# Kernel optimization log

Measured on AMD Instinct MI355X. Metric: run time of the kernel, lower is better.

The kernel has to match this reference:

```python
import jax, jax.numpy as jnp
import numpy as np

B, M, D, H = 2, 2048, 1024, 16
DH = D // H            # 64 head dim
R_ATTN = 512           # rank of q/k/v SVD factors
FFN_D = 2048           # GEGLU inner dim; Wi out = 2*FFN_D
R_FFN = 1024           # rank of FFN SVD factors
ROPE_BASE = 10000.0
LN_EPS = 1e-5


def _layernorm(x, g, b):
    mu = jnp.mean(x, axis=-1, keepdims=True)
    var = jnp.mean(jnp.square(x - mu), axis=-1, keepdims=True)
    return (x - mu) * jax.lax.rsqrt(var + LN_EPS) * g + b


def _rotate_half(x):
    x1, x2 = jnp.split(x, 2, axis=-1)
    return jnp.concatenate((-x2, x1), axis=-1)


def _rope_cos_sin(m, dh, dtype):
    inv_freq = 1.0 / (ROPE_BASE ** (jnp.arange(0, dh, 2, dtype=jnp.float32) / dh))
    freqs = jnp.arange(m, dtype=jnp.float32)[:, None] * inv_freq[None, :]  # [M, dh/2]
    emb = jnp.concatenate((freqs, freqs), axis=-1)  # [M, dh]
    return jnp.cos(emb).astype(dtype), jnp.sin(emb).astype(dtype)


def setup_inputs() -> dict:
    key = jax.random.key(0)
    ks = iter(jax.random.split(key, 32))
    rn = lambda shape, s: jax.random.normal(next(ks), shape, jnp.float32) * s
    w = 0.02
    return {
        'hidden_states': rn((B, M, D), 1.0),
        'ln1_g': jnp.ones((D,), jnp.float32), 'ln1_b': jnp.zeros((D,), jnp.float32),
        'Uq': rn((D, R_ATTN), w), 'Vq': rn((R_ATTN, D), w), 'bq': rn((D,), w),
        'Uk': rn((D, R_ATTN), w), 'Vk': rn((R_ATTN, D), w), 'bk': rn((D,), w),
        'Uv': rn((D, R_ATTN), w), 'Vv': rn((R_ATTN, D), w), 'bv': rn((D,), w),
        'Wo': rn((D, D), w), 'bo': rn((D,), w),  # dense attn out proj, torch [out,in]
        'ln2_g': jnp.ones((D,), jnp.float32), 'ln2_b': jnp.zeros((D,), jnp.float32),
        'U1': rn((D, R_FFN), w), 'V1': rn((R_FFN, 2 * FFN_D), w), 'b1': rn((2 * FFN_D,), w),
        'U2': rn((FFN_D, R_FFN), w), 'V2': rn((R_FFN, D), w), 'b2': rn((D,), w),
    }


def reference(hidden_states, ln1_g, ln1_b, Uq, Vq, bq, Uk, Vk, bk, Uv, Vv, bv,
              Wo, bo, ln2_g, ln2_b, U1, V1, b1, U2, V2, b2):
    x = hidden_states
    xn = _layernorm(x, ln1_g, ln1_b)
    # low-rank QKV: y = (x @ U) @ V + b
    q = (xn @ Uq) @ Vq + bq
    k = (xn @ Uk) @ Vk + bk
    v = (xn @ Uv) @ Vv + bv
    to_bhmd = lambda t: t.reshape(B, M, H, DH).transpose(0, 2, 1, 3)
    q, k, v = to_bhmd(q), to_bhmd(k), to_bhmd(v)
    cos, sin = _rope_cos_sin(M, DH, q.dtype)  # [M, DH]
    q = q * cos + _rotate_half(q) * sin
    k = k * cos + _rotate_half(k) * sin
    scale = 1.0 / np.sqrt(DH)
    scores = jnp.einsum('bhmd,bhnd->bhmn', q, k) * scale  # [B,H,M,M]
    attn = jax.nn.softmax(scores, axis=-1)
    out = jnp.einsum('bhmn,bhnd->bhmd', attn, v)
    out = out.transpose(0, 2, 1, 3).reshape(B, M, D)
    x = x + out @ Wo.T + bo
    # low-rank GEGLU FFN
    xn2 = _layernorm(x, ln2_g, ln2_b)
    z = (xn2 @ U1) @ V1 + b1  # [B,M,2*FFN_D]
    z1, z2 = jnp.split(z, 2, axis=-1)
    h = jax.nn.gelu(z1, approximate=True) * z2  # GEGLU, tanh approx
    y = (h @ U2) @ V2 + b2
    return x + y
```

## Files before the change

kernel.cpp:

```cpp
#include <hip/hip_runtime.h>


typedef unsigned short u16;
typedef unsigned int u32;
typedef u16 u16x8 __attribute__((ext_vector_type(8)));
typedef __bf16 bf16x8 __attribute__((ext_vector_type(8)));
typedef float f32x4 __attribute__((ext_vector_type(4)));

__device__ __forceinline__ u16 f2bf(float f) {
    u32 u = __builtin_bit_cast(u32, f);
    u += 0x7fff + ((u >> 16) & 1);
    return (u16)(u >> 16);
}
__device__ __forceinline__ float bf2f(u16 h) {
    u32 u = ((u32)h) << 16;
    return __builtin_bit_cast(float, u);
}
__device__ __forceinline__ u32 packbf(float a, float b) {
    return __builtin_amdgcn_perm(__builtin_bit_cast(u32, b),
                                 __builtin_bit_cast(u32, a), 0x07060302u);
}

__device__ __forceinline__ void gload16(const void* g, void* l) {
    __builtin_amdgcn_global_load_lds(
        (const __attribute__((address_space(1))) void*)g,
        (__attribute__((address_space(3))) void*)l, 16, 0, 0);
}

#define MB 1048576u
#define OFF_UQKVT (0*MB)
#define OFF_VQKVT (3*MB)
#define OFF_WOB   (6*MB)
#define OFF_U1T   (8*MB)
#define OFF_V1TP  (10*MB)
#define OFF_U2T   (18*MB)
#define OFF_V2T   (22*MB)
#define OFF_BQKV  (24*MB)
#define OFF_B1P   (24*MB + 16384u)
#define OFF_XN    (25*MB)
#define OFF_TBUF  (33*MB)
#define OFF_QB    (45*MB)
#define OFF_KB    (53*MB)
#define OFF_HB    (45*MB)
#define OFF_VTB   (61*MB)
#define OFF_OB    (69*MB)
#define OFF_X2    (93*MB)

__global__ __launch_bounds__(256) void prep_kernel(
    const float* __restrict__ Uq, const float* __restrict__ Uk,
    const float* __restrict__ Uv, const float* __restrict__ Vq,
    const float* __restrict__ Vk, const float* __restrict__ Vv,
    const float* __restrict__ Wo, const float* __restrict__ U1,
    const float* __restrict__ V1, const float* __restrict__ U2,
    const float* __restrict__ V2,
    const float* __restrict__ bq, const float* __restrict__ bk,
    const float* __restrict__ bv, const float* __restrict__ b1,
    u16* __restrict__ UQKVT, u16* __restrict__ VQKVT, u16* __restrict__ WOB,
    u16* __restrict__ U1T, u16* __restrict__ V1TP, u16* __restrict__ U2T,
    u16* __restrict__ V2T, float* __restrict__ BQKV, float* __restrict__ B1P)
{
    __shared__ float tile[32][33];
    int bid = blockIdx.x;

    if (bid >= 12288) {
        int id = (bid - 12288) * 256 + threadIdx.x;
        if (id < 3072) {
            float v = (id < 1024) ? bq[id] : (id < 2048 ? bk[id - 1024] : bv[id - 2048]);
            BQKV[id] = v;
        }
        int g = id >> 5, s = id & 31;
        B1P[id] = b1[(s < 16) ? (g*16 + s) : (2048 + g*16 + (s - 16))];
        return;
    }
    if (bid >= 11264) {
        int i4 = ((bid - 11264) * 256 + threadIdx.x) * 4;
        float4 v = *(const float4*)(Wo + i4);
        u16 tmp[4] = {f2bf(v.x), f2bf(v.y), f2bf(v.z), f2bf(v.w)};
        *(uint2*)(WOB + i4) = *(const uint2*)tmp;
        return;
    }

    const float* src; u16* dst; int K, N, src_ld, nx; bool gg = false;
    if (bid < 3072) {
        int t = bid / 512; bid -= t * 512;
        if (t < 3) { src = t==0 ? Uq : (t==1 ? Uk : Uv);
                     dst = UQKVT + t * 512*1024; K = 1024; N = 512; src_ld = 512; nx = 16; }
        else { int z = t - 3; src = z==0 ? Vq : (z==1 ? Vk : Vv);
               dst = VQKVT + z * 524288; K = 512; N = 1024; src_ld = 1024; nx = 32; }
    } else if (bid < 4096)  { src = U1; dst = U1T;  K = 1024; N = 1024; src_ld = 1024; nx = 32;  bid -= 3072; }
    else if (bid < 8192)    { src = V1; dst = V1TP; K = 1024; N = 4096; src_ld = 4096; nx = 128; bid -= 4096; gg = true; }
    else if (bid < 10240)   { src = U2; dst = U2T;  K = 2048; N = 1024; src_ld = 1024; nx = 32;  bid -= 8192; }
    else                    { src = V2; dst = V2T;  K = 1024; N = 1024; src_ld = 1024; nx = 32;  bid -= 10240; }

    int tx = threadIdx.x & 31, ty = threadIdx.x >> 5;
    int n0 = (bid % nx) * 32, k0 = (bid / nx) * 32;
    int srccol;
    if (gg) { int g = n0 >> 5; srccol = (tx < 16) ? (g*16 + tx) : (2048 + g*16 + (tx - 16)); }
    else srccol = n0 + tx;
    for (int i = 0; i < 4; i++)
        tile[ty + i*8][tx] = src[(size_t)(k0 + ty + i*8) * src_ld + srccol];
    __syncthreads();
    for (int i = 0; i < 4; i++)
        dst[(size_t)(n0 + ty + i*8) * K + k0 + tx] = f2bf(tile[tx][ty + i*8]);
}

__global__ __launch_bounds__(256) void ln_kernel(
    const float* __restrict__ x, const float* __restrict__ g,
    const float* __restrict__ bta, u16* __restrict__ out)
{
    int w = threadIdx.x >> 6, lane = threadIdx.x & 63;
    int row = blockIdx.x * 4 + w;
    const float* xr = x + (size_t)row * 1024;
    float vals[16];
    float s = 0.f, s2 = 0.f;
    #pragma unroll
    for (int ii = 0; ii < 16; ii++) {
        float v = xr[lane + ii*64];
        vals[ii] = v; s += v; s2 += v * v;
    }
    #pragma unroll
    for (int off = 1; off < 64; off <<= 1) {
        s  += __shfl_xor(s, off);
        s2 += __shfl_xor(s2, off);
    }
    float mu = s * (1.f/1024.f);
    float var = s2 * (1.f/1024.f) - mu * mu;
    float rs = rsqrtf(var + 1e-5f);
    #pragma unroll
    for (int ii = 0; ii < 16; ii++) {
        int col = lane + ii*64;
        out[(size_t)row * 1024 + col] = f2bf((vals[ii] - mu) * rs * g[col] + bta[col]);
    }
}

__global__ __launch_bounds__(256) void gemm_bt_kernel(
    const u16* __restrict__ A, int lda, const u16* __restrict__ Bt,
    void* __restrict__ Cout, int ldc, const float* __restrict__ bias,
    const float* __restrict__ resid, int Kdim, int mode)
{
    __shared__ u16 As[2][4096];
    __shared__ u16 Bs[2][4096];
    int tid = threadIdx.x;
    int m0 = blockIdx.y * 128, n0 = blockIdx.x * 128;
    int w = tid >> 6, lane = tid & 63, quad = lane >> 4, l15 = lane & 15;
    int wm = (w >> 1) * 64, wn = (w & 1) * 64;
    int sr = tid >> 2, sc8 = (tid & 3) * 8;

    f32x4 acc[4][4] = {};

    const u16* Ap = A  + (size_t)(m0 + sr) * lda  + sc8;
    const u16* Bp = Bt + (size_t)(n0 + sr) * Kdim + sc8;

    #define GSTAGE(buf, koff) do {                                        \
        gload16(Ap + (koff),                     &As[buf][tid * 8]);      \
        gload16(Ap + (koff) + (size_t)64 * lda,  &As[buf][2048 + tid*8]); \
        gload16(Bp + (koff),                     &Bs[buf][tid * 8]);      \
        gload16(Bp + (koff) + (size_t)64 * Kdim, &Bs[buf][2048 + tid*8]); \
    } while (0)

    GSTAGE(0, 0);
    __syncthreads();

    for (int k0 = 0; k0 < Kdim; k0 += 32) {
        int cur = (k0 >> 5) & 1;
        if (k0 + 32 < Kdim) GSTAGE(cur ^ 1, k0 + 32);
        const u16* Asc = As[cur];
        const u16* Bsc = Bs[cur];
        bf16x8 af[4], bfr[4];
        #pragma unroll
        for (int i = 0; i < 4; i++)
            af[i] = *(const bf16x8*)&Asc[(wm + i*16 + l15) * 32 + quad * 8];
        #pragma unroll
        for (int j = 0; j < 4; j++)
            bfr[j] = *(const bf16x8*)&Bsc[(wn + j*16 + l15) * 32 + quad * 8];
        #pragma unroll
        for (int i = 0; i < 4; i++)
            #pragma unroll
            for (int j = 0; j < 4; j++)
                acc[i][j] = __builtin_amdgcn_mfma_f32_16x16x32_bf16(af[i], bfr[j], acc[i][j], 0, 0, 0);
        __syncthreads();
    }
    #undef GSTAGE

    if (mode == 2) {
        u16* hb = (u16*)Cout;
        #pragma unroll
        for (int i = 0; i < 4; i++) {
            int row = m0 + wm + i*16 + quad*4;
            #pragma unroll
            for (int p = 0; p < 2; p++) {
                int colz = n0 + wn + p*32 + l15;
                float bz1 = bias[colz], bz2 = bias[colz + 16];
                int hcol = ((n0 + wn) >> 1) + p*16 + l15;
                #pragma unroll
                for (int r = 0; r < 4; r++) {
                    float z1 = acc[i][2*p][r] + bz1;
                    float z2 = acc[i][2*p+1][r] + bz2;
                    float uu = 0.7978845608028654f * (z1 + 0.044715f * z1 * z1 * z1);
                    float e = __expf(2.f * uu);
                    float th = (e - 1.f) / (e + 1.f);
                    float hv = 0.5f * z1 * (1.f + th) * z2;
                    hb[(size_t)(row + r) * ldc + hcol] = f2bf(hv);
                }
            }
        }
        return;
    }
    #pragma unroll
    for (int i = 0; i < 4; i++) {
        int row = m0 + wm + i*16 + quad*4;
        #pragma unroll
        for (int j = 0; j < 4; j++) {
            int col = n0 + wn + j*16 + l15;
            float bv = bias ? bias[col] : 0.f;
            #pragma unroll
            for (int r = 0; r < 4; r++) {
                float v = acc[i][j][r] + bv;
                size_t idx = (size_t)(row + r) * ldc + col;
                if (mode == 0) ((float*)Cout)[idx] = v + resid[idx];
                else           ((u16*)Cout)[idx] = f2bf(v);
            }
        }
    }
}

__global__ __launch_bounds__(256) void gemm_bt64_kernel(
    const u16* __restrict__ A, int lda, const u16* __restrict__ Bt,
    void* __restrict__ Cout, int ldc, const float* __restrict__ bias,
    const float* __restrict__ resid, int Kdim, int mode)
{
    __shared__ u16 As[2][4096];
    __shared__ u16 Bs[2][2048];
    int tid = threadIdx.x;
    int m0 = blockIdx.y * 128, n0 = blockIdx.x * 64;
    int w = tid >> 6, lane = tid & 63, quad = lane >> 4, l15 = lane & 15;
    int wm = (w >> 1) * 64, wn = (w & 1) * 32;
    int sr = tid >> 2, sc8 = (tid & 3) * 8;

    f32x4 acc[4][2] = {};

    const u16* Ap = A  + (size_t)(m0 + sr) * lda  + sc8;
    const u16* Bp = Bt + (size_t)(n0 + sr) * Kdim + sc8;

    #define GSTAGE64(buf, koff) do {                                       \
        gload16(Ap + (koff),                     &As[buf][tid * 8]);       \
        gload16(Ap + (koff) + (size_t)64 * lda,  &As[buf][2048 + tid*8]);  \
        gload16(Bp + (koff),                     &Bs[buf][tid * 8]);       \
    } while (0)

    GSTAGE64(0, 0);
    __syncthreads();

    for (int k0 = 0; k0 < Kdim; k0 += 32) {
        int cur = (k0 >> 5) & 1;
        if (k0 + 32 < Kdim) GSTAGE64(cur ^ 1, k0 + 32);
        const u16* Asc = As[cur];
        const u16* Bsc = Bs[cur];
        bf16x8 af[4], bfr[2];
        #pragma unroll
        for (int i = 0; i < 4; i++)
            af[i] = *(const bf16x8*)&Asc[(wm + i*16 + l15) * 32 + quad * 8];
        #pragma unroll
        for (int j = 0; j < 2; j++)
            bfr[j] = *(const bf16x8*)&Bsc[(wn + j*16 + l15) * 32 + quad * 8];
        #pragma unroll
        for (int i = 0; i < 4; i++)
            #pragma unroll
            for (int j = 0; j < 2; j++)
                acc[i][j] = __builtin_amdgcn_mfma_f32_16x16x32_bf16(af[i], bfr[j], acc[i][j], 0, 0, 0);
        __syncthreads();
    }
    #undef GSTAGE64

    #pragma unroll
    for (int i = 0; i < 4; i++) {
        int row = m0 + wm + i*16 + quad*4;
        #pragma unroll
        for (int j = 0; j < 2; j++) {
            int col = n0 + wn + j*16 + l15;
            float bv = bias ? bias[col] : 0.f;
            #pragma unroll
            for (int r = 0; r < 4; r++) {
                float v = acc[i][j][r] + bv;
                size_t idx = (size_t)(row + r) * ldc + col;
                if (mode == 0) ((float*)Cout)[idx] = v + resid[idx];
                else           ((u16*)Cout)[idx] = f2bf(v);
            }
        }
    }
}

__global__ __launch_bounds__(256) void qkv2_kernel(
    const u16* __restrict__ T, const u16* __restrict__ Vw,
    const float* __restrict__ bqkv, u16* __restrict__ qout,
    u16* __restrict__ kout, u16* __restrict__ vtout)
{
    __shared__ u16 As[2][4096];
    __shared__ u16 Bs[2][4096];
    int tid = threadIdx.x;
    int z = blockIdx.z;
    int m0 = blockIdx.y * 128, n0 = blockIdx.x * 128;
    int w = tid >> 6, lane = tid & 63, quad = lane >> 4, l15 = lane & 15;
    int wm = (w >> 1) * 64, wn = (w & 1) * 64;
    int sr = tid >> 2, sc8 = (tid & 3) * 8;

    f32x4 acc[4][4] = {};

    const u16* Ap = T  + (size_t)z * 512 + (size_t)(m0 + sr) * 1536 + sc8;
    const u16* Bp = Vw + (size_t)z * 512 * 1024 + (size_t)(n0 + sr) * 512 + sc8;

    #define QSTAGE(buf, koff) do {                                        \
        gload16(Ap + (koff),                     &As[buf][tid * 8]);      \
        gload16(Ap + (koff) + (size_t)64 * 1536, &As[buf][2048 + tid*8]); \
        gload16(Bp + (koff),                     &Bs[buf][tid * 8]);      \
        gload16(Bp + (koff) + (size_t)64 * 512,  &Bs[buf][2048 + tid*8]); \
    } while (0)

    QSTAGE(0, 0);
    __syncthreads();

    for (int k0 = 0; k0 < 512; k0 += 32) {
        int cur = (k0 >> 5) & 1;
        if (k0 + 32 < 512) QSTAGE(cur ^ 1, k0 + 32);
        const u16* Asc = As[cur];
        const u16* Bsc = Bs[cur];
        bf16x8 af[4], bfr[4];
        #pragma unroll
        for (int i = 0; i < 4; i++)
            af[i] = *(const bf16x8*)&Asc[(wm + i*16 + l15) * 32 + quad * 8];
        #pragma unroll
        for (int j = 0; j < 4; j++)
            bfr[j] = *(const bf16x8*)&Bsc[(wn + j*16 + l15) * 32 + quad * 8];
        #pragma unroll
        for (int i = 0; i < 4; i++)
            #pragma unroll
            for (int j = 0; j < 4; j++)
                acc[i][j] = __builtin_amdgcn_mfma_f32_16x16x32_bf16(af[i], bfr[j], acc[i][j], 0, 0, 0);
        __syncthreads();
    }
    #undef QSTAGE

    const float* bias = bqkv + z * 1024;
    if (z < 2) {
        u16* Ob = z ? kout : qout;
        float qscale = z ? 1.f : 0.18033688011112042f;
        #pragma unroll
        for (int i = 0; i < 4; i++) {
            int row0 = m0 + wm + i*16 + quad*4;
            #pragma unroll
            for (int j = 0; j < 2; j++) {
                int col = n0 + wn + j*16 + l15;
                float bj = bias[col], bj2 = bias[col + 32];
                float invf = exp2f((float)(col & 31) * -0.4152410118609203f);
                #pragma unroll
                for (int r = 0; r < 4; r++) {
                    int t = row0 + r;
                    float fr = (float)(t & 2047) * invf;
                    float sn, cs;
                    __sincosf(fr, &sn, &cs);
                    sn *= qscale; cs *= qscale;
                    float v1 = acc[i][j][r] + bj;
                    float v2 = acc[i][j+2][r] + bj2;
                    Ob[(size_t)t * 1024 + col]      = f2bf(v1 * cs - v2 * sn);
                    Ob[(size_t)t * 1024 + col + 32] = f2bf(v2 * cs + v1 * sn);
                }
            }
        }
    } else {
        int bb = m0 >> 11;
        #pragma unroll
        for (int i = 0; i < 4; i++) {
            int row0 = m0 + wm + i*16 + quad*4;
            #pragma unroll
            for (int j = 0; j < 4; j++) {
                int col = n0 + wn + j*16 + l15;
                float bj = bias[col];
                u16 pack[4];
                #pragma unroll
                for (int r = 0; r < 4; r++) pack[r] = f2bf(acc[i][j][r] + bj);
                size_t dst = ((size_t)(bb * 16 + (col >> 6)) * 64 + (col & 63)) * 2048 + (row0 & 2047);
                *(uint2*)&vtout[dst] = *(const uint2*)pack;
            }
        }
    }
}

__global__ __launch_bounds__(256) void attn_kernel(
    const u16* __restrict__ Q, const u16* __restrict__ K,
    const u16* __restrict__ Vt, u16* __restrict__ O)
{
    __shared__ u16 Ks[2][64 * 64];
    __shared__ u16 Vs[2][64 * 64];
    __shared__ u16 Ps[128 * 72];
    int tid = threadIdx.x;
    int bh = blockIdx.x;
    int b = bh >> 4, h = bh & 15;
    int m0 = blockIdx.y * 128;
    int w = tid >> 6, lane = tid & 63, quad = lane >> 4, l15 = lane & 15;
    int wm = w * 32;
    size_t qkbase = (size_t)b * 2048 * 1024 + h * 64;
    const u16* Vg = Vt + (size_t)bh * 64 * 2048;

    bf16x8 qf[2][2];
    #pragma unroll
    for (int i = 0; i < 2; i++)
        #pragma unroll
        for (int ks = 0; ks < 2; ks++)
            qf[i][ks] = *(const bf16x8*)(Q + qkbase +
                (size_t)(m0 + wm + i*16 + l15) * 1024 + ks*32 + quad*8);

    f32x4 oacc[2][4] = {};
    float lsum[2] = {};

    int r0 = tid >> 3, p = tid & 7;
    int c0 = (p ^ (r0 & 7)) * 8;
    int xsw = l15 & 7;

    #define STAGE(buf, key0) do {                                               \
        gload16(K + qkbase + (size_t)((key0) + r0) * 1024 + c0,                 \
                &Ks[buf][r0 * 64 + p * 8]);                                     \
        gload16(K + qkbase + (size_t)((key0) + r0 + 32) * 1024 + c0,            \
                &Ks[buf][(r0 + 32) * 64 + p * 8]);                              \
        gload16(Vg + (size_t)r0 * 2048 + (key0) + c0,                           \
                &Vs[buf][r0 * 64 + p * 8]);                                     \
        gload16(Vg + (size_t)(r0 + 32) * 2048 + (key0) + c0,                    \
                &Vs[buf][(r0 + 32) * 64 + p * 8]);                              \
    } while (0)

    STAGE(0, 0);
    __syncthreads();

    for (int kt = 0; kt < 32; kt++) {
        int cur = kt & 1;
        if (kt < 31) STAGE(cur ^ 1, (kt + 1) * 64);
        const u16* Ksc = Ks[cur];
        const u16* Vsc = Vs[cur];

        f32x4 sacc[4][2] = {};
        #pragma unroll
        for (int ks = 0; ks < 2; ks++) {
            bf16x8 kf[4];
            #pragma unroll
            for (int jj = 0; jj < 4; jj++)
                kf[jj] = *(const bf16x8*)&Ksc[(jj*16 + l15) * 64 + (((ks*4 + quad) ^ xsw) * 8)];
            #pragma unroll
            for (int jj = 0; jj < 4; jj++)
                #pragma unroll
                for (int i = 0; i < 2; i++)
                    sacc[jj][i] = __builtin_amdgcn_mfma_f32_16x16x32_bf16(kf[jj], qf[i][ks], sacc[jj][i], 0, 0, 0);
        }

        #pragma unroll
        for (int i = 0; i < 2; i++) {
            int prow = (wm + i*16 + l15) * 72 + quad*4;
            #pragma unroll
            for (int jj = 0; jj < 4; jj++) {
                float p0 = __builtin_amdgcn_exp2f(sacc[jj][i][0]);
                float p1 = __builtin_amdgcn_exp2f(sacc[jj][i][1]);
                float p2 = __builtin_amdgcn_exp2f(sacc[jj][i][2]);
                float p3 = __builtin_amdgcn_exp2f(sacc[jj][i][3]);
                lsum[i] += (p0 + p1) + (p2 + p3);
                uint2 pk; pk.x = packbf(p0, p1); pk.y = packbf(p2, p3);
                *(uint2*)&Ps[prow + jj*16] = pk;
            }
        }

        #pragma unroll
        for (int ks = 0; ks < 2; ks++) {
            bf16x8 pf[2], vf[4];
            #pragma unroll
            for (int i = 0; i < 2; i++)
                pf[i] = *(const bf16x8*)&Ps[(wm + i*16 + l15) * 72 + ks*32 + quad*8];
            #pragma unroll
            for (int j = 0; j < 4; j++)
                vf[j] = *(const bf16x8*)&Vsc[(j*16 + l15) * 64 + (((ks*4 + quad) ^ xsw) * 8)];
            #pragma unroll
            for (int i = 0; i < 2; i++)
                #pragma unroll
                for (int j = 0; j < 4; j++)
                    oacc[i][j] = __builtin_amdgcn_mfma_f32_16x16x32_bf16(pf[i], vf[j], oacc[i][j], 0, 0, 0);
        }
        __syncthreads();
    }
    #undef STAGE

    float inv[2][4];
    #pragma unroll
    for (int i = 0; i < 2; i++) {
        float s = lsum[i];
        s += __shfl_xor(s, 16);
        s += __shfl_xor(s, 32);
        #pragma unroll
        for (int r = 0; r < 4; r++)
            inv[i][r] = 1.f / __shfl(s, (lane & 48) | (quad*4 + r));
    }
    #pragma unroll
    for (int i = 0; i < 2; i++)
        #pragma unroll
        for (int r = 0; r < 4; r++) {
            int row = m0 + wm + i*16 + quad*4 + r;
            #pragma unroll
            for (int j = 0; j < 4; j++)
                O[qkbase + (size_t)row * 1024 + j*16 + l15] = f2bf(oacc[i][j][r] * inv[i][r]);
        }
}

extern "C" void kernel_launch(void* const* d_in, const int* in_sizes, int n_in,
                              void* d_out, int out_size, void* d_ws, size_t ws_size,
                              hipStream_t stream) {
    (void)in_sizes; (void)n_in; (void)out_size; (void)ws_size;
    const float* x     = (const float*)d_in[0];
    const float* ln1_g = (const float*)d_in[1];
    const float* ln1_b = (const float*)d_in[2];
    const float* Uq    = (const float*)d_in[3];
    const float* Vq    = (const float*)d_in[4];
    const float* bq    = (const float*)d_in[5];
    const float* Uk    = (const float*)d_in[6];
    const float* Vk    = (const float*)d_in[7];
    const float* bk    = (const float*)d_in[8];
    const float* Uv    = (const float*)d_in[9];
    const float* Vv    = (const float*)d_in[10];
    const float* bv    = (const float*)d_in[11];
    const float* Wo    = (const float*)d_in[12];
    const float* bo    = (const float*)d_in[13];
    const float* ln2_g = (const float*)d_in[14];
    const float* ln2_b = (const float*)d_in[15];
    const float* U1    = (const float*)d_in[16];
    const float* V1    = (const float*)d_in[17];
    const float* b1    = (const float*)d_in[18];
    const float* U2    = (const float*)d_in[19];
    const float* V2    = (const float*)d_in[20];
    const float* b2    = (const float*)d_in[21];
    float* out = (float*)d_out;
    char* ws = (char*)d_ws;

    u16* UQKVT = (u16*)(ws + OFF_UQKVT);
    u16* VQKVT = (u16*)(ws + OFF_VQKVT);
    u16* WOB   = (u16*)(ws + OFF_WOB);
    u16* U1T   = (u16*)(ws + OFF_U1T);
    u16* V1TP  = (u16*)(ws + OFF_V1TP);
    u16* U2T   = (u16*)(ws + OFF_U2T);
    u16* V2T   = (u16*)(ws + OFF_V2T);
    float* BQKV = (float*)(ws + OFF_BQKV);
    float* B1P  = (float*)(ws + OFF_B1P);
    u16* xn  = (u16*)(ws + OFF_XN);
    u16* tbuf= (u16*)(ws + OFF_TBUF);
    u16* qb  = (u16*)(ws + OFF_QB);
    u16* kb  = (u16*)(ws + OFF_KB);
    u16* vtb = (u16*)(ws + OFF_VTB);
    u16* ob  = (u16*)(ws + OFF_OB);
    u16* hb  = (u16*)(ws + OFF_HB);
    float* x2 = (float*)(ws + OFF_X2);

    prep_kernel<<<12304, 256, 0, stream>>>(
        Uq, Uk, Uv, Vq, Vk, Vv, Wo, U1, V1, U2, V2, bq, bk, bv, b1,
        UQKVT, VQKVT, WOB, U1T, V1TP, U2T, V2T, BQKV, B1P);

    ln_kernel<<<1024, 256, 0, stream>>>(x, ln1_g, ln1_b, xn);

    gemm_bt64_kernel<<<dim3(24, 32), 256, 0, stream>>>(xn, 1024, UQKVT, tbuf, 1536,
                                                       nullptr, nullptr, 1024, 1);
    qkv2_kernel<<<dim3(8, 32, 3), 256, 0, stream>>>(tbuf, VQKVT, BQKV, qb, kb, vtb);

    attn_kernel<<<dim3(32, 16), 256, 0, stream>>>(qb, kb, vtb, ob);

    gemm_bt64_kernel<<<dim3(16, 32), 256, 0, stream>>>(ob, 1024, WOB, x2, 1024,
                                                       bo, x, 1024, 0);
    ln_kernel<<<1024, 256, 0, stream>>>(x2, ln2_g, ln2_b, xn);

    gemm_bt64_kernel<<<dim3(16, 32), 256, 0, stream>>>(xn, 1024, U1T, tbuf, 1024,
                                                       nullptr, nullptr, 1024, 1);
    gemm_bt_kernel<<<dim3(32, 32), 256, 0, stream>>>(tbuf, 1024, V1TP, hb, 2048,
                                                     B1P, nullptr, 1024, 2);
    gemm_bt64_kernel<<<dim3(16, 32), 256, 0, stream>>>(hb, 2048, U2T, tbuf, 1024,
                                                       nullptr, nullptr, 2048, 1);
    gemm_bt64_kernel<<<dim3(16, 32), 256, 0, stream>>>(tbuf, 1024, V2T, out, 1024,
                                                       b2, x2, 1024, 0);
}
```

Measured before the change: 421.7 us.

## Replace GEGLU V1 GEMM with 256x256-tile, 8-wave, swizzled, phase-pipelined kernel

The 128x128 GEGLU up-projection GEMM is replaced by a 256x256 tile kernel with 512 threads and BK=64. It uses XOR-swizzled LDS layout, split half-tile global-to-LDS staging interleaved with four MFMA phases, explicit barriers and waitcnts, and setprio around the MFMA blocks. The V1/b1 interleave is changed to 64-column groups to match the new per-wave gate/up column mapping. The goal is more data reuse per LDS byte and better overlap of loads with MFMA, at the cost of large LDS use (128KB) and only 256 blocks.

```diff
diff --git a/kernel.cpp b/kernel.cpp
--- a/kernel.cpp
+++ b/kernel.cpp
@@ -68,8 +68,8 @@
             float v = (id < 1024) ? bq[id] : (id < 2048 ? bk[id - 1024] : bv[id - 2048]);
             BQKV[id] = v;
         }
-        int g = id >> 5, s = id & 31;
-        B1P[id] = b1[(s < 16) ? (g*16 + s) : (2048 + g*16 + (s - 16))];
+        int g = id >> 7, q = id & 127;
+        B1P[id] = b1[(q < 64) ? (g*64 + q) : (2048 + g*64 + (q - 64))];
         return;
     }
     if (bid >= 11264) {
@@ -95,7 +95,8 @@
     int tx = threadIdx.x & 31, ty = threadIdx.x >> 5;
     int n0 = (bid % nx) * 32, k0 = (bid / nx) * 32;
     int srccol;
-    if (gg) { int g = n0 >> 5; srccol = (tx < 16) ? (g*16 + tx) : (2048 + g*16 + (tx - 16)); }
+    if (gg) { int p = n0 + tx; int g = p >> 7, q = p & 127;
+              srccol = (q < 64) ? (g*64 + q) : (2048 + g*64 + (q - 64)); }
     else srccol = n0 + tx;
     for (int i = 0; i < 4; i++)
         tile[ty + i*8][tx] = src[(size_t)(k0 + ty + i*8) * src_ld + srccol];
@@ -133,92 +134,164 @@
     }
 }
 
-__global__ __launch_bounds__(256) void gemm_bt_kernel(
-    const u16* __restrict__ A, int lda, const u16* __restrict__ Bt,
-    void* __restrict__ Cout, int ldc, const float* __restrict__ bias,
-    const float* __restrict__ resid, int Kdim, int mode)
+__global__ __launch_bounds__(512) void gemm256_geglu_kernel(
+    const u16* __restrict__ A, const u16* __restrict__ Bt,
+    u16* __restrict__ hb, const float* __restrict__ bias, int Kdim)
 {
-    __shared__ u16 As[2][4096];
-    __shared__ u16 Bs[2][4096];
+    __shared__ u16 As[2][16384];
+    __shared__ u16 Bs[2][16384];
     int tid = threadIdx.x;
-    int m0 = blockIdx.y * 128, n0 = blockIdx.x * 128;
+    int m0 = blockIdx.y * 256, n0 = blockIdx.x * 256;
     int w = tid >> 6, lane = tid & 63, quad = lane >> 4, l15 = lane & 15;
-    int wm = (w >> 1) * 64, wn = (w & 1) * 64;
-    int sr = tid >> 2, sc8 = (tid & 3) * 8;
-
-    f32x4 acc[4][4] = {};
-
-    const u16* Ap = A  + (size_t)(m0 + sr) * lda  + sc8;
-    const u16* Bp = Bt + (size_t)(n0 + sr) * Kdim + sc8;
-
-    #define GSTAGE(buf, koff) do {                                        \
-        gload16(Ap + (koff),                     &As[buf][tid * 8]);      \
-        gload16(Ap + (koff) + (size_t)64 * lda,  &As[buf][2048 + tid*8]); \
-        gload16(Bp + (koff),                     &Bs[buf][tid * 8]);      \
-        gload16(Bp + (koff) + (size_t)64 * Kdim, &Bs[buf][2048 + tid*8]); \
-    } while (0)
-
-    GSTAGE(0, 0);
-    __syncthreads();
-
-    for (int k0 = 0; k0 < Kdim; k0 += 32) {
-        int cur = (k0 >> 5) & 1;
-        if (k0 + 32 < Kdim) GSTAGE(cur ^ 1, k0 + 32);
-        const u16* Asc = As[cur];
-        const u16* Bsc = Bs[cur];
-        bf16x8 af[4], bfr[4];
-        #pragma unroll
-        for (int i = 0; i < 4; i++)
-            af[i] = *(const bf16x8*)&Asc[(wm + i*16 + l15) * 32 + quad * 8];
-        #pragma unroll
-        for (int j = 0; j < 4; j++)
-            bfr[j] = *(const bf16x8*)&Bsc[(wn + j*16 + l15) * 32 + quad * 8];
-        #pragma unroll
-        for (int i = 0; i < 4; i++)
-            #pragma unroll
-            for (int j = 0; j < 4; j++)
-                acc[i][j] = __builtin_amdgcn_mfma_f32_16x16x32_bf16(af[i], bfr[j], acc[i][j], 0, 0, 0);
-        __syncthreads();
-    }
-    #undef GSTAGE
-
-    if (mode == 2) {
-        u16* hb = (u16*)Cout;
+    int wr = (w >> 2) * 16, wc = (w & 3) * 16;
+    int xsw = l15 & 7;
+    int s0 = (quad ^ xsw) * 8, s1 = s0 ^ 32;
+
+    int srow = tid >> 3;
+    int scol = ((tid & 7) ^ (srow & 7)) * 8;
+    const u16* Ap = A  + (size_t)(m0 + srow) * Kdim + scol;
+    const u16* Bp = Bt + (size_t)(n0 + srow) * Kdim + scol;
+
+    int abase = (wr + l15) * 64;
+    int bbase = (wc + l15) * 64;
+
+    f32x4 acc[8][4] = {};
+
+#define STG_A(buf, t, h) do {                                                      \
+    gload16(Ap + (size_t)(t)*64 + (size_t)((h)*128     )*Kdim,                     \
+            &As[buf][(h)*8192 + tid*8]);                                           \
+    gload16(Ap + (size_t)(t)*64 + (size_t)((h)*128 + 64)*Kdim,                     \
+            &As[buf][(h)*8192 + 4096 + tid*8]);                                    \
+} while (0)
+#define STG_B(buf, t, h) do {                                                      \
+    gload16(Bp + (size_t)(t)*64 + (size_t)((h)*128     )*Kdim,                     \
+            &Bs[buf][(h)*8192 + tid*8]);                                           \
+    gload16(Bp + (size_t)(t)*64 + (size_t)((h)*128 + 64)*Kdim,                     \
+            &Bs[buf][(h)*8192 + 4096 + tid*8]);                                    \
+} while (0)
+#define SB()  __builtin_amdgcn_sched_barrier(0)
+#define BAR() do { SB(); __builtin_amdgcn_s_barrier(); SB(); } while (0)
+#define WAITL() do { asm volatile("s_waitcnt lgkmcnt(0)" ::: "memory"); SB(); } while (0)
+
+    int nt = Kdim >> 6;
+
+    STG_A(0, 0, 0); STG_B(0, 0, 0); STG_A(0, 0, 1); STG_B(0, 0, 1);
+    STG_A(1, 1, 0); STG_B(1, 1, 0);
+    asm volatile("s_waitcnt vmcnt(4)" ::: "memory");
+    __builtin_amdgcn_s_barrier();
+    SB();
+
+    bf16x8 af[4][2], bfl[2][2], bfh[2][2];
+
+    for (int t = 0; t < nt; ++t) {
+        int buf = t & 1, nbuf = buf ^ 1;
+        const u16* Asc = As[buf];
+        const u16* Bsc = Bs[buf];
+
         #pragma unroll
         for (int i = 0; i < 4; i++) {
-            int row = m0 + wm + i*16 + quad*4;
-            #pragma unroll
-            for (int p = 0; p < 2; p++) {
-                int colz = n0 + wn + p*32 + l15;
-                float bz1 = bias[colz], bz2 = bias[colz + 16];
-                int hcol = ((n0 + wn) >> 1) + p*16 + l15;
-                #pragma unroll
-                for (int r = 0; r < 4; r++) {
-                    float z1 = acc[i][2*p][r] + bz1;
-                    float z2 = acc[i][2*p+1][r] + bz2;
-                    float uu = 0.7978845608028654f * (z1 + 0.044715f * z1 * z1 * z1);
-                    float e = __expf(2.f * uu);
-                    float th = (e - 1.f) / (e + 1.f);
-                    float hv = 0.5f * z1 * (1.f + th) * z2;
-                    hb[(size_t)(row + r) * ldc + hcol] = f2bf(hv);
-                }
-            }
-        }
-        return;
-    }
-    #pragma unroll
-    for (int i = 0; i < 4; i++) {
-        int row = m0 + wm + i*16 + quad*4;
-        #pragma unroll
-        for (int j = 0; j < 4; j++) {
-            int col = n0 + wn + j*16 + l15;
-            float bv = bias ? bias[col] : 0.f;
+            af[i][0] = *(const bf16x8*)&Asc[abase + i*2048 + s0];
+            af[i][1] = *(const bf16x8*)&Asc[abase + i*2048 + s1];
+        }
+        #pragma unroll
+        for (int j = 0; j < 2; j++) {
+            bfl[j][0] = *(const bf16x8*)&Bsc[bbase + j*4096 + s0];
+            bfl[j][1] = *(const bf16x8*)&Bsc[bbase + j*4096 + s1];
+        }
+        if (t + 1 < nt) STG_A(nbuf, t+1, 1);
+        BAR();
+        WAITL();
+        __builtin_amdgcn_s_setprio(1);
+        #pragma unroll
+        for (int i = 0; i < 4; i++)
+            #pragma unroll
+            for (int j = 0; j < 2; j++) {
+                acc[i][j] = __builtin_amdgcn_mfma_f32_16x16x32_bf16(af[i][0], bfl[j][0], acc[i][j], 0, 0, 0);
+                acc[i][j] = __builtin_amdgcn_mfma_f32_16x16x32_bf16(af[i][1], bfl[j][1], acc[i][j], 0, 0, 0);
+            }
+        __builtin_amdgcn_s_setprio(0);
+        BAR();
+
+        #pragma unroll
+        for (int j = 0; j < 2; j++) {
+            bfh[j][0] = *(const bf16x8*)&Bsc[bbase + 8192 + j*4096 + s0];
+            bfh[j][1] = *(const bf16x8*)&Bsc[bbase + 8192 + j*4096 + s1];
+        }
+        if (t + 1 < nt) STG_B(nbuf, t+1, 1);
+        BAR();
+        WAITL();
+        __builtin_amdgcn_s_setprio(1);
+        #pragma unroll
+        for (int i = 0; i < 4; i++)
+            #pragma unroll
+            for (int j = 0; j < 2; j++) {
+                acc[i][2+j] = __builtin_amdgcn_mfma_f32_16x16x32_bf16(af[i][0], bfh[j][0], acc[i][2+j], 0, 0, 0);
+                acc[i][2+j] = __builtin_amdgcn_mfma_f32_16x16x32_bf16(af[i][1], bfh[j][1], acc[i][2+j], 0, 0, 0);
+            }
+        __builtin_amdgcn_s_setprio(0);
+        BAR();
+
+        #pragma unroll
+        for (int i = 0; i < 4; i++) {
+            af[i][0] = *(const bf16x8*)&Asc[abase + 8192 + i*2048 + s0];
+            af[i][1] = *(const bf16x8*)&Asc[abase + 8192 + i*2048 + s1];
+        }
+        if (t + 2 < nt) STG_A(buf, t+2, 0);
+        BAR();
+        WAITL();
+        __builtin_amdgcn_s_setprio(1);
+        #pragma unroll
+        for (int i = 0; i < 4; i++)
+            #pragma unroll
+            for (int j = 0; j < 2; j++) {
+                acc[4+i][j] = __builtin_amdgcn_mfma_f32_16x16x32_bf16(af[i][0], bfl[j][0], acc[4+i][j], 0, 0, 0);
+                acc[4+i][j] = __builtin_amdgcn_mfma_f32_16x16x32_bf16(af[i][1], bfl[j][1], acc[4+i][j], 0, 0, 0);
+            }
+        __builtin_amdgcn_s_setprio(0);
+        BAR();
+
+        if (t + 2 < nt) STG_B(buf, t+2, 0);
+        BAR();
+        __builtin_amdgcn_s_setprio(1);
+        #pragma unroll
+        for (int i = 0; i < 4; i++)
+            #pragma unroll
+            for (int j = 0; j < 2; j++) {
+                acc[4+i][2+j] = __builtin_amdgcn_mfma_f32_16x16x32_bf16(af[i][0], bfh[j][0], acc[4+i][2+j], 0, 0, 0);
+                acc[4+i][2+j] = __builtin_amdgcn_mfma_f32_16x16x32_bf16(af[i][1], bfh[j][1], acc[4+i][2+j], 0, 0, 0);
+            }
+        __builtin_amdgcn_s_setprio(0);
+        if (t + 1 < nt) {
+            SB();
+            if (t + 2 < nt) asm volatile("s_waitcnt vmcnt(4)" ::: "memory");
+            else            asm volatile("s_waitcnt vmcnt(0)" ::: "memory");
+            __builtin_amdgcn_s_barrier();
+            SB();
+        }
+    }
+#undef STG_A
+#undef STG_B
+#undef SB
+#undef BAR
+#undef WAITL
+
+    #pragma unroll
+    for (int mi = 0; mi < 8; mi++) {
+        int row = m0 + wr + mi*32 + quad*4;
+        #pragma unroll
+        for (int p = 0; p < 2; p++) {
+            int c1 = n0 + p*128 + wc + l15;
+            float bz1 = bias[c1], bz2 = bias[c1 + 64];
+            int hcol = (n0 >> 1) + p*64 + wc + l15;
             #pragma unroll
             for (int r = 0; r < 4; r++) {
-                float v = acc[i][j][r] + bv;
-                size_t idx = (size_t)(row + r) * ldc + col;
-                if (mode == 0) ((float*)Cout)[idx] = v + resid[idx];
-                else           ((u16*)Cout)[idx] = f2bf(v);
+                float z1 = acc[mi][2*p][r] + bz1;
+                float z2 = acc[mi][2*p+1][r] + bz2;
+                float uu = 0.7978845608028654f * (z1 + 0.044715f * z1 * z1 * z1);
+                float e = __expf(2.f * uu);
+                float th = (e - 1.f) / (e + 1.f);
+                float hv = 0.5f * z1 * (1.f + th) * z2;
+                hb[(size_t)(row + r) * 2048 + hcol] = f2bf(hv);
             }
         }
     }
@@ -570,8 +643,7 @@
 
     gemm_bt64_kernel<<<dim3(16, 32), 256, 0, stream>>>(xn, 1024, U1T, tbuf, 1024,
                                                        nullptr, nullptr, 1024, 1);
-    gemm_bt_kernel<<<dim3(32, 32), 256, 0, stream>>>(tbuf, 1024, V1TP, hb, 2048,
-                                                     B1P, nullptr, 1024, 2);
+    gemm256_geglu_kernel<<<dim3(16, 16), 512, 0, stream>>>(tbuf, V1TP, hb, B1P, 1024);
     gemm_bt64_kernel<<<dim3(16, 32), 256, 0, stream>>>(hb, 2048, U2T, tbuf, 1024,
                                                        nullptr, nullptr, 2048, 1);
     gemm_bt64_kernel<<<dim3(16, 32), 256, 0, stream>>>(tbuf, 1024, V2T, out, 1024,
```

Result: faster. 408.9 us (-3.0%).
